# Kernel tuning notes

Measured on AMD Instinct MI355X. Metric: run time of the kernel, lower is better.

Reference implementation:

```python
import jax, jax.numpy as jnp
import numpy as np

N = 50000      # nodes
E = 800000     # edges (avg degree 16)
G = 256        # graphs in batch
IN = 128       # in_channels
H = 256        # hidden_channels
L = 4          # num_layers


def setup_inputs() -> dict:
    key = jax.random.key(0)
    ks = jax.random.split(key, 16)
    x = jax.random.normal(ks[0], (N, IN), dtype=jnp.float32)
    edge_index = jax.random.randint(ks[1], (2, E), 0, N, dtype=jnp.int64)
    batch = jnp.sort(jax.random.randint(ks[2], (N,), 0, G, dtype=jnp.int64))
    s_in = 1.0 / np.sqrt(IN)
    s_h = 1.0 / np.sqrt(H)
    return {
        "x": x,
        "edge_index": edge_index,
        "batch": batch,
        "w1_0": jax.random.normal(ks[3], (IN, H), jnp.float32) * s_in,
        "b1_0": jnp.zeros((H,), jnp.float32),
        "w2_0": jax.random.normal(ks[4], (H, H), jnp.float32) * s_h,
        "b2_0": jnp.zeros((H,), jnp.float32),
        "w1s": jax.random.normal(ks[5], (L - 1, H, H), jnp.float32) * s_h,
        "b1s": jnp.zeros((L - 1, H), jnp.float32),
        "w2s": jax.random.normal(ks[6], (L - 1, H, H), jnp.float32) * s_h,
        "b2s": jnp.zeros((L - 1, H), jnp.float32),
    }


def reference(x, edge_index, batch, w1_0, b1_0, w2_0, b2_0, w1s, b1s, w2s, b2s):
    n_nodes = x.shape[0]
    src, dst = edge_index[0], edge_index[1]

    def gin_layer(h, w1, b1, w2, b2):
        # scatter-add neighbor aggregation: out[i] = sum_{(j->i)} h[j]
        agg = jax.ops.segment_sum(h[src], dst, num_segments=n_nodes)
        z = h + agg  # GIN with eps = 0: (1+eps)*x + aggr
        z = jax.nn.relu(z @ w1 + b1) @ w2 + b2  # MLP: Linear-ReLU-Linear
        return jax.nn.relu(z)  # outer F.relu in forward

    h = gin_layer(x, w1_0, b1_0, w2_0, b2_0)
    for i in range(L - 1):  # small fixed layer loop
        h = gin_layer(h, w1s[i], b1s[i], w2s[i], b2s[i])

    # global_add_pool: per-graph segment sum -> [G, H]
    return jax.ops.segment_sum(h, batch, num_segments=G)
```

## Files before the change

### kernel.cpp

```cpp
#include <hip/hip_runtime.h>
#include <hip/hip_bf16.h>

#define NN 50000
#define NE 800000
#define NG 256
#define CIN 128
#define CH 256
#define CAP 64

typedef unsigned short u16;
typedef unsigned int u32;
typedef unsigned char u8;
typedef __attribute__((ext_vector_type(8))) short short8;
typedef __attribute__((ext_vector_type(8))) unsigned short ushort8;
typedef __attribute__((ext_vector_type(4))) float f32x4;

__device__ __forceinline__ float bf2f(u16 u) { return __uint_as_float(((u32)u) << 16); }
__device__ __forceinline__ u16 f2bf(float f) {
    u32 u = __float_as_uint(f);
    return (u16)((u + 0x7fffu + ((u >> 16) & 1u)) >> 16);
}

__global__ void k_prep(const float* __restrict__ x, u16* __restrict__ xb,
                       const float* __restrict__ w1_0, const float* __restrict__ w2_0,
                       const float* __restrict__ w1s, const float* __restrict__ w2s,
                       u16* __restrict__ Wp, int* __restrict__ deg,
                       float* __restrict__ outf,
                       float* __restrict__ S0, float* __restrict__ S1) {
    int t = blockIdx.x * 256 + threadIdx.x;
    if (t < NN) deg[t] = 0;
    if (t < NG * CH) outf[t] = 0.f;
    if (t < CIN) xb[(size_t)NN * CIN + t] = 0;
    if (t == 0) { S0[NN] = 0.f; S1[NN] = 0.f; }
    if (t < NN * CIN / 4) {
        float4 v = ((const float4*)x)[t];
        ushort4 o; o.x = f2bf(v.x); o.y = f2bf(v.y); o.z = f2bf(v.z); o.w = f2bf(v.w);
        ((ushort4*)xb)[t] = o;
    }
    if (t < CIN * CH + 7 * CH * CH) {
        const float* Wsrc; int rem;
        if (t < CIN * CH) { Wsrc = w1_0; rem = t; }
        else {
            int o = t - CIN * CH;
            int m = o >> 16; rem = o & 65535;
            Wsrc = (m == 0) ? w2_0
                 : (m <= 3) ? w1s + (size_t)(m - 1) * 65536
                            : w2s + (size_t)(m - 4) * 65536;
        }
        int j = rem & 7, lane = (rem >> 3) & 63, nt = (rem >> 9) & 15, kb = rem >> 13;
        int k = kb * 32 + ((lane >> 4) << 3) + j;
        int nc = nt * 16 + (lane & 15);
        Wp[t] = f2bf(Wsrc[k * CH + nc]);
    }
}

__global__ __launch_bounds__(256) void k_build(const int* __restrict__ dst,
                                               const int* __restrict__ src,
                                               int* __restrict__ deg,
                                               u16* __restrict__ colu) {
    int t = blockIdx.x * 256 + threadIdx.x;
    int e0 = t * 2;
    if (e0 < NE) {
        int2 d2 = *(const int2*)(dst + e0);
        int2 s2 = *(const int2*)(src + e0);
        int p0 = atomicAdd(&deg[d2.x], 1);
        int p1 = atomicAdd(&deg[d2.y], 1);
        colu[d2.x * CAP + p0] = (u16)s2.x;
        colu[d2.y * CAP + p1] = (u16)s2.y;
    }
}

#define ZS 264
template <int K1, bool QIN, bool QOUT, bool POOL>
__global__ __launch_bounds__(256, 6) void k_layer(const u16* __restrict__ G,
                                                  const int* __restrict__ deg,
                                                  const u16* __restrict__ colu,
                                                  const u8* __restrict__ Qin,
                                                  const float* __restrict__ Sin,
                                                  const u16* __restrict__ Wp1,
                                                  const float* __restrict__ b1,
                                                  const u16* __restrict__ Wp2,
                                                  const float* __restrict__ b2,
                                                  u16* __restrict__ out,
                                                  u8* __restrict__ Qout,
                                                  float* __restrict__ Sout,
                                                  const int* __restrict__ batchp,
                                                  float* __restrict__ outf) {
    __shared__ __align__(16) u16 zs[32 * ZS];
    const int tid = threadIdx.x;
    const int wave = tid >> 6, lane = tid & 63;
    const int quad = lane >> 4, l16 = lane & 15;
    const int m0 = blockIdx.x * 32;

    if (!QIN) {
        constexpr int LPR = K1 / 8;
        constexpr int RPG = 64 / LPR;
        const int sub = lane / LPR;
        const int c0 = (lane % LPR) * 8;
        for (int g = 0; g < 8; g += RPG) {
            int lr = wave * 8 + g + sub;
            int r = m0 + lr; if (r >= NN) r = NN - 1;
            const u16* base = G + c0;
            float a[8];
            ushort8 sv = *(const ushort8*)(base + (size_t)r * K1);
#pragma unroll
            for (int i = 0; i < 8; i++) a[i] = bf2f(sv[i]);
            int dg = deg[r];
            const u16* cb = colu + r * CAP;
            for (int e = 0; e < dg; e += 8) {
                ushort8 cv = *(const ushort8*)(cb + e);
                int idx[8];
#pragma unroll
                for (int u = 0; u < 8; u++)
                    idx[u] = (e + u < dg) ? (int)cv[u] : NN;
                ushort8 v[8];
#pragma unroll
                for (int u = 0; u < 8; u++)
                    v[u] = *(const ushort8*)(base + (size_t)idx[u] * K1);
#pragma unroll
                for (int u = 0; u < 8; u++)
#pragma unroll
                    for (int i = 0; i < 8; i++) a[i] += bf2f(v[u][i]);
            }
            ushort8 o;
#pragma unroll
            for (int i = 0; i < 8; i++) o[i] = f2bf(a[i]);
            *(ushort8*)(zs + lr * ZS + c0) = o;
        }
    } else {
        const int sub = lane >> 4;
        const int c0 = (lane & 15) * 16;
        for (int g = 0; g < 8; g += 4) {
            int lr = wave * 8 + g + sub;
            int r = m0 + lr; if (r >= NN) r = NN - 1;
            float a[16];
            const u16* sp = G + (size_t)r * CH + c0;
            ushort8 s0v = *(const ushort8*)sp;
            ushort8 s1v = *(const ushort8*)(sp + 8);
#pragma unroll
            for (int i = 0; i < 8; i++) { a[i] = bf2f(s0v[i]); a[8 + i] = bf2f(s1v[i]); }
            int dg = deg[r];
            const u16* cb = colu + r * CAP;
            for (int e = 0; e < dg; e += 4) {
                ushort4 cv = *(const ushort4*)(cb + e);
                int idx[4] = {(int)cv.x, (int)cv.y, (int)cv.z, (int)cv.w};
#pragma unroll
                for (int u = 0; u < 4; u++)
                    if (e + u >= dg) idx[u] = NN;
                uint4 qv[4]; float sc[4];
#pragma unroll
                for (int u = 0; u < 4; u++) {
                    qv[u] = *(const uint4*)(Qin + (size_t)idx[u] * CH + c0);
                    sc[u] = Sin[idx[u]];
                }
#pragma unroll
                for (int u = 0; u < 4; u++) {
#pragma unroll
                    for (int d = 0; d < 4; d++) {
                        u32 w = ((const u32*)&qv[u])[d];
                        a[d * 4 + 0] += sc[u] * (float)(w & 0xffu);
                        a[d * 4 + 1] += sc[u] * (float)((w >> 8) & 0xffu);
                        a[d * 4 + 2] += sc[u] * (float)((w >> 16) & 0xffu);
                        a[d * 4 + 3] += sc[u] * (float)(w >> 24);
                    }
                }
            }
            ushort8 o0, o1;
#pragma unroll
            for (int i = 0; i < 8; i++) { o0[i] = f2bf(a[i]); o1[i] = f2bf(a[8 + i]); }
            *(ushort8*)(zs + lr * ZS + c0) = o0;
            *(ushort8*)(zs + lr * ZS + c0 + 8) = o1;
        }
    }
    __syncthreads();

    f32x4 acc[2][4];
#pragma unroll
    for (int ri = 0; ri < 2; ri++)
#pragma unroll
        for (int nj = 0; nj < 4; nj++) acc[ri][nj] = (f32x4){0.f, 0.f, 0.f, 0.f};

    const u16* w1b = Wp1 + (wave * 4) * 512 + lane * 8;
    const u16* w2b = Wp2 + (wave * 4) * 512 + lane * 8;
    constexpr int KB1 = K1 / 32;
    short8 b_cur[4], b_nxt[4];
#pragma unroll
    for (int nj = 0; nj < 4; nj++) b_cur[nj] = *(const short8*)(w1b + nj * 512);

#pragma unroll
    for (int kb = 0; kb < KB1; kb++) {
        int kn = (kb + 1 < KB1) ? (kb + 1) : kb;
#pragma unroll
        for (int nj = 0; nj < 4; nj++)
            b_nxt[nj] = *(const short8*)(w1b + kn * 8192 + nj * 512);
        short8 a[2];
#pragma unroll
        for (int ri = 0; ri < 2; ri++)
            a[ri] = *(const short8*)(zs + (ri * 16 + l16) * ZS + kb * 32 + quad * 8);
#pragma unroll
        for (int nj = 0; nj < 4; nj++)
#pragma unroll
            for (int ri = 0; ri < 2; ri++)
                acc[ri][nj] = __builtin_amdgcn_mfma_f32_16x16x32_bf16(a[ri], b_cur[nj], acc[ri][nj], 0, 0, 0);
#pragma unroll
        for (int nj = 0; nj < 4; nj++) b_cur[nj] = b_nxt[nj];
    }

    short8 b2_cur[4];
#pragma unroll
    for (int nj = 0; nj < 4; nj++) b2_cur[nj] = *(const short8*)(w2b + nj * 512);

    __syncthreads();

#pragma unroll
    for (int nj = 0; nj < 4; nj++) {
        int cc = wave * 64 + nj * 16 + l16;
        float bv = b1[cc];
#pragma unroll
        for (int ri = 0; ri < 2; ri++) {
            f32x4 v = acc[ri][nj];
#pragma unroll
            for (int j = 0; j < 4; j++)
                zs[(ri * 16 + quad * 4 + j) * ZS + cc] = f2bf(fmaxf(v[j] + bv, 0.f));
        }
    }
    __syncthreads();

#pragma unroll
    for (int ri = 0; ri < 2; ri++)
#pragma unroll
        for (int nj = 0; nj < 4; nj++) acc[ri][nj] = (f32x4){0.f, 0.f, 0.f, 0.f};

#pragma unroll
    for (int kb = 0; kb < 8; kb++) {
        int kn = (kb + 1 < 8) ? (kb + 1) : kb;
#pragma unroll
        for (int nj = 0; nj < 4; nj++)
            b_nxt[nj] = *(const short8*)(w2b + kn * 8192 + nj * 512);
        short8 a[2];
#pragma unroll
        for (int ri = 0; ri < 2; ri++)
            a[ri] = *(const short8*)(zs + (ri * 16 + l16) * ZS + kb * 32 + quad * 8);
#pragma unroll
        for (int nj = 0; nj < 4; nj++)
#pragma unroll
            for (int ri = 0; ri < 2; ri++)
                acc[ri][nj] = __builtin_amdgcn_mfma_f32_16x16x32_bf16(a[ri], b2_cur[nj], acc[ri][nj], 0, 0, 0);
#pragma unroll
        for (int nj = 0; nj < 4; nj++) b2_cur[nj] = b_nxt[nj];
    }
    __syncthreads();

#pragma unroll
    for (int nj = 0; nj < 4; nj++) {
        int cc = wave * 64 + nj * 16 + l16;
        float bv = b2[cc];
#pragma unroll
        for (int ri = 0; ri < 2; ri++) {
            f32x4 v = acc[ri][nj];
#pragma unroll
            for (int j = 0; j < 4; j++)
                zs[(ri * 16 + quad * 4 + j) * ZS + cc] = f2bf(fmaxf(v[j] + bv, 0.f));
        }
    }
    __syncthreads();

    if (!POOL) {
        int row = tid >> 3, cb = (tid & 7) * 32;
        int r = m0 + row;
        if (r < NN) {
            uint4* dst = (uint4*)(out + (size_t)r * CH + cb);
            const u16* srcp = zs + row * ZS + cb;
#pragma unroll
            for (int c = 0; c < 4; c++) dst[c] = *(const uint4*)(srcp + c * 8);
            if (QOUT) {
                float vloc[32]; float mx = 0.f;
#pragma unroll
                for (int c = 0; c < 32; c++) { vloc[c] = bf2f(srcp[c]); mx = fmaxf(mx, vloc[c]); }
                mx = fmaxf(mx, __shfl_xor(mx, 1));
                mx = fmaxf(mx, __shfl_xor(mx, 2));
                mx = fmaxf(mx, __shfl_xor(mx, 4));
                float inv = mx > 0.f ? 255.f / mx : 0.f;
                u32 qw[8];
#pragma unroll
                for (int d = 0; d < 8; d++) {
                    u32 q0 = (u32)(vloc[d * 4 + 0] * inv + 0.5f);
                    u32 q1 = (u32)(vloc[d * 4 + 1] * inv + 0.5f);
                    u32 q2 = (u32)(vloc[d * 4 + 2] * inv + 0.5f);
                    u32 q3 = (u32)(vloc[d * 4 + 3] * inv + 0.5f);
                    qw[d] = q0 | (q1 << 8) | (q2 << 16) | (q3 << 24);
                }
                uint4* qdst = (uint4*)(Qout + (size_t)r * CH + cb);
                qdst[0] = *(const uint4*)&qw[0];
                qdst[1] = *(const uint4*)&qw[4];
                if ((tid & 7) == 0) Sout[r] = mx * (1.f / 255.f);
            }
        }
    } else {
        int c = tid;
        float acc2 = 0.f;
        int cur_g = batchp[m0];
        for (int row = 0; row < 32; row++) {
            int r = m0 + row;
            if (r >= NN) break;
            int g = batchp[r];
            if (g != cur_g) {
                atomicAdd(&outf[cur_g * CH + c], acc2);
                acc2 = 0.f; cur_g = g;
            }
            acc2 += bf2f(zs[row * ZS + c]);
        }
        atomicAdd(&outf[cur_g * CH + c], acc2);
    }
}

extern "C" void kernel_launch(void* const* d_in, const int* in_sizes, int n_in,
                              void* d_out, int out_size, void* d_ws, size_t ws_size,
                              hipStream_t stream) {
    const float* x     = (const float*)d_in[0];
    const int*   ei    = (const int*)d_in[1];
    const int*   batch = (const int*)d_in[2];
    const float* w1_0  = (const float*)d_in[3];
    const float* b1_0  = (const float*)d_in[4];
    const float* w2_0  = (const float*)d_in[5];
    const float* b2_0  = (const float*)d_in[6];
    const float* w1s   = (const float*)d_in[7];
    const float* b1s   = (const float*)d_in[8];
    const float* w2s   = (const float*)d_in[9];
    const float* b2s   = (const float*)d_in[10];
    float* out = (float*)d_out;

    char* p = (char*)d_ws;
    u16* Hb  = (u16*)p; p += (size_t)(NN + 1) * CH * 2;
    u16* Tb  = (u16*)p; p += (size_t)(NN + 1) * CH * 2;
    u16* xb  = (u16*)p; p += (size_t)(NN + 1) * CIN * 2;
    u16* WpA = (u16*)p; p += (size_t)(CIN * CH + 7 * CH * CH) * 2;
    int* deg = (int*)p; p += (size_t)NN * 4;
    u16* colu= (u16*)p; p += (size_t)NN * CAP * 2;
    u8*  Q0  = (u8*)p;  p += (size_t)(NN + 1) * CH;
    u8*  Q1  = (u8*)p;  p += (size_t)(NN + 1) * CH;
    float* S0 = (float*)p; p += (size_t)(NN + 1) * 4;
    float* S1 = (float*)p; p += (size_t)(NN + 1) * 4;

    u16* Wp1_0 = WpA;
    u16* Wp2_0 = Wp1_0 + CIN * CH;
    u16* Wp1sA = Wp2_0 + CH * CH;
    u16* Wp2sA = Wp1sA + 3 * CH * CH;

    const int* srcv = ei;
    const int* dstv = ei + NE;

    hipLaunchKernelGGL(k_prep, dim3((NN * CIN / 4 + 255) / 256), dim3(256), 0, stream,
                       x, xb, w1_0, w2_0, w1s, w2s, WpA, deg, out, S0, S1);

    hipLaunchKernelGGL(k_build, dim3((NE / 2 + 255) / 256), dim3(256), 0, stream,
                       dstv, srcv, deg, colu);

    int layerBlocks = (NN + 31) / 32;

    hipLaunchKernelGGL((k_layer<128, false, true, false>), dim3(layerBlocks), dim3(256), 0, stream,
                       xb, deg, colu, (const u8*)nullptr, (const float*)nullptr,
                       Wp1_0, b1_0, Wp2_0, b2_0, Hb, Q0, S0, batch, out);
    hipLaunchKernelGGL((k_layer<256, true, true, false>), dim3(layerBlocks), dim3(256), 0, stream,
                       Hb, deg, colu, Q0, S0,
                       Wp1sA, b1s, Wp2sA, b2s, Tb, Q1, S1, batch, out);
    hipLaunchKernelGGL((k_layer<256, true, true, false>), dim3(layerBlocks), dim3(256), 0, stream,
                       Tb, deg, colu, Q1, S1,
                       Wp1sA + (size_t)CH * CH, b1s + CH,
                       Wp2sA + (size_t)CH * CH, b2s + CH, Hb, Q0, S0, batch, out);
    hipLaunchKernelGGL((k_layer<256, true, false, true>), dim3(layerBlocks), dim3(256), 0, stream,
                       Hb, deg, colu, Q0, S0,
                       Wp1sA + (size_t)2 * CH * CH, b1s + 2 * CH,
                       Wp2sA + (size_t)2 * CH * CH, b2s + 2 * CH,
                       (u16*)nullptr, (u8*)nullptr, (float*)nullptr, batch, out);
}
```

Before: 393.8 us.

## Bucket neighbor lists by source range and prefetch slices for cache locality

Adds a k_sort pass that reorders each node's neighbor list into 8 source-node partitions and stores packed per-partition prefix counts. The gather loops in k_layer then walk the partitions in lockstep across all blocks, while each block prefetches a slice of the upcoming partitions' feature rows. The goal is to keep the random gathers within a cache-resident window instead of touching the whole feature table at once. This costs an extra kernel launch, redundant prefetch loads with hardcoded offsets, and processes two rows interleaved per lane, which raises register pressure.

Measured after the change: 561.3 us. 1.43x slower.

```diff
diff --git a/kernel.cpp b/kernel.cpp
--- a/kernel.cpp
+++ b/kernel.cpp
@@ -7,18 +7,32 @@
 #define CIN 128
 #define CH 256
 #define CAP 64
+#define NPART 8
 
 typedef unsigned short u16;
 typedef unsigned int u32;
 typedef unsigned char u8;
+typedef unsigned long long u64;
 typedef __attribute__((ext_vector_type(8))) short short8;
 typedef __attribute__((ext_vector_type(8))) unsigned short ushort8;
 typedef __attribute__((ext_vector_type(4))) float f32x4;
+typedef __attribute__((ext_vector_type(4))) unsigned int u32x4;
 
 __device__ __forceinline__ float bf2f(u16 u) { return __uint_as_float(((u32)u) << 16); }
 __device__ __forceinline__ u16 f2bf(float f) {
     u32 u = __float_as_uint(f);
     return (u16)((u + 0x7fffu + ((u >> 16) & 1u)) >> 16);
+}
+
+__device__ __forceinline__ void pf_slice(const u8* base, int p, int islice, int tid) {
+    size_t off = (size_t)p * 1600000 + (size_t)islice * 8192 + (size_t)tid * 32;
+    const size_t lim = 12800224;
+    if (off > lim) off = lim;
+    const u32x4* q = (const u32x4*)(base + off);
+    u32x4 v0 = q[0];
+    u32x4 v1 = q[1];
+    u32 s = v0[0] ^ v0[1] ^ v0[2] ^ v0[3] ^ v1[0] ^ v1[1] ^ v1[2] ^ v1[3];
+    asm volatile("" :: "v"(s));
 }
 
 __global__ void k_prep(const float* __restrict__ x, u16* __restrict__ xb,
@@ -70,11 +84,35 @@
     }
 }
 
+__global__ __launch_bounds__(256) void k_sort(const int* __restrict__ deg,
+                                              u16* __restrict__ colu,
+                                              u64* __restrict__ cnt) {
+    const int lane = threadIdx.x & 63;
+    const int r = blockIdx.x * 4 + (threadIdx.x >> 6);
+    if (r >= NN) return;
+    const int dg = deg[r];
+    const bool valid = lane < dg;
+    u16 id = colu[r * CAP + lane];
+    u32 p = valid ? (u32)(((u64)id * 687195ull) >> 32) : 8u;
+    const u64 lm = (1ull << lane) - 1;
+    int base = 0, mypos = 0;
+    u64 packed = 0;
+#pragma unroll
+    for (u32 q = 0; q < 8; q++) {
+        u64 m = __ballot(p == q);
+        if (p == q) mypos = base + __popcll(m & lm);
+        base += __popcll(m);
+        packed |= ((u64)(u32)base) << (q * 8);
+    }
+    if (valid) colu[r * CAP + mypos] = id;
+    if (lane == 0) cnt[r] = packed;
+}
+
 #define ZS 264
 template <int K1, bool QIN, bool QOUT, bool POOL>
 __global__ __launch_bounds__(256, 6) void k_layer(const u16* __restrict__ G,
-                                                  const int* __restrict__ deg,
                                                   const u16* __restrict__ colu,
+                                                  const u64* __restrict__ cnt,
                                                   const u8* __restrict__ Qin,
                                                   const float* __restrict__ Sin,
                                                   const u16* __restrict__ Wp1,
@@ -91,83 +129,122 @@
     const int wave = tid >> 6, lane = tid & 63;
     const int quad = lane >> 4, l16 = lane & 15;
     const int m0 = blockIdx.x * 32;
+    const int islice = (int)blockIdx.x >> 3;
 
     if (!QIN) {
         constexpr int LPR = K1 / 8;
         constexpr int RPG = 64 / LPR;
         const int sub = lane / LPR;
         const int c0 = (lane % LPR) * 8;
-        for (int g = 0; g < 8; g += RPG) {
-            int lr = wave * 8 + g + sub;
+        int ee[2]; u64 cn[2];
+        const u16* cbp[2];
+        float a[2][8];
+#pragma unroll
+        for (int b = 0; b < 2; b++) {
+            int lr = wave * 8 + b * RPG + sub;
             int r = m0 + lr; if (r >= NN) r = NN - 1;
-            const u16* base = G + c0;
-            float a[8];
-            ushort8 sv = *(const ushort8*)(base + (size_t)r * K1);
-#pragma unroll
-            for (int i = 0; i < 8; i++) a[i] = bf2f(sv[i]);
-            int dg = deg[r];
-            const u16* cb = colu + r * CAP;
-            for (int e = 0; e < dg; e += 8) {
-                ushort8 cv = *(const ushort8*)(cb + e);
-                int idx[8];
-#pragma unroll
-                for (int u = 0; u < 8; u++)
-                    idx[u] = (e + u < dg) ? (int)cv[u] : NN;
-                ushort8 v[8];
-#pragma unroll
-                for (int u = 0; u < 8; u++)
-                    v[u] = *(const ushort8*)(base + (size_t)idx[u] * K1);
-#pragma unroll
-                for (int u = 0; u < 8; u++)
-#pragma unroll
-                    for (int i = 0; i < 8; i++) a[i] += bf2f(v[u][i]);
+            ee[b] = 0; cbp[b] = colu + r * CAP; cn[b] = cnt[r];
+            ushort8 sv = *(const ushort8*)(G + (size_t)r * K1 + c0);
+#pragma unroll
+            for (int i = 0; i < 8; i++) a[b][i] = bf2f(sv[i]);
+        }
+        const u8* pfb = (const u8*)G;
+        pf_slice(pfb, 0, islice, tid);
+        pf_slice(pfb, 1, islice, tid);
+        const u16* base = G + c0;
+        for (int p = 0; p < 8; p++) {
+            if (p < 6) pf_slice(pfb, p + 2, islice, tid);
+#pragma unroll
+            for (int b = 0; b < 2; b++) {
+                const int limit = (int)((cn[b] >> (p * 8)) & 0xffu);
+                const int dgt = (int)(cn[b] >> 56);
+                while (ee[b] < limit) {
+                    int e = ee[b];
+                    ushort8 cv = *(const ushort8*)(cbp[b] + e);
+                    int idx[8];
+#pragma unroll
+                    for (int u = 0; u < 8; u++)
+                        idx[u] = (e + u < dgt) ? (int)cv[u] : NN;
+                    ushort8 v[8];
+#pragma unroll
+                    for (int u = 0; u < 8; u++)
+                        v[u] = *(const ushort8*)(base + (size_t)idx[u] * K1);
+#pragma unroll
+                    for (int u = 0; u < 8; u++)
+#pragma unroll
+                        for (int i = 0; i < 8; i++) a[b][i] += bf2f(v[u][i]);
+                    ee[b] = e + 8;
+                }
             }
+        }
+#pragma unroll
+        for (int b = 0; b < 2; b++) {
+            int lr = wave * 8 + b * RPG + sub;
             ushort8 o;
 #pragma unroll
-            for (int i = 0; i < 8; i++) o[i] = f2bf(a[i]);
+            for (int i = 0; i < 8; i++) o[i] = f2bf(a[b][i]);
             *(ushort8*)(zs + lr * ZS + c0) = o;
         }
     } else {
         const int sub = lane >> 4;
         const int c0 = (lane & 15) * 16;
-        for (int g = 0; g < 8; g += 4) {
-            int lr = wave * 8 + g + sub;
+        int ee[2]; u64 cn[2];
+        const u16* cbp[2];
+        float a[2][16];
+#pragma unroll
+        for (int b = 0; b < 2; b++) {
+            int lr = wave * 8 + b * 4 + sub;
             int r = m0 + lr; if (r >= NN) r = NN - 1;
-            float a[16];
+            ee[b] = 0; cbp[b] = colu + r * CAP; cn[b] = cnt[r];
             const u16* sp = G + (size_t)r * CH + c0;
             ushort8 s0v = *(const ushort8*)sp;
             ushort8 s1v = *(const ushort8*)(sp + 8);
 #pragma unroll
-            for (int i = 0; i < 8; i++) { a[i] = bf2f(s0v[i]); a[8 + i] = bf2f(s1v[i]); }
-            int dg = deg[r];
-            const u16* cb = colu + r * CAP;
-            for (int e = 0; e < dg; e += 4) {
-                ushort4 cv = *(const ushort4*)(cb + e);
-                int idx[4] = {(int)cv.x, (int)cv.y, (int)cv.z, (int)cv.w};
-#pragma unroll
-                for (int u = 0; u < 4; u++)
-                    if (e + u >= dg) idx[u] = NN;
-                uint4 qv[4]; float sc[4];
-#pragma unroll
-                for (int u = 0; u < 4; u++) {
-                    qv[u] = *(const uint4*)(Qin + (size_t)idx[u] * CH + c0);
-                    sc[u] = Sin[idx[u]];
-                }
-#pragma unroll
-                for (int u = 0; u < 4; u++) {
-#pragma unroll
-                    for (int d = 0; d < 4; d++) {
-                        u32 w = ((const u32*)&qv[u])[d];
-                        a[d * 4 + 0] += sc[u] * (float)(w & 0xffu);
-                        a[d * 4 + 1] += sc[u] * (float)((w >> 8) & 0xffu);
-                        a[d * 4 + 2] += sc[u] * (float)((w >> 16) & 0xffu);
-                        a[d * 4 + 3] += sc[u] * (float)(w >> 24);
+            for (int i = 0; i < 8; i++) { a[b][i] = bf2f(s0v[i]); a[b][8 + i] = bf2f(s1v[i]); }
+        }
+        const u8* pfb = Qin;
+        pf_slice(pfb, 0, islice, tid);
+        pf_slice(pfb, 1, islice, tid);
+        for (int p = 0; p < 8; p++) {
+            if (p < 6) pf_slice(pfb, p + 2, islice, tid);
+#pragma unroll
+            for (int b = 0; b < 2; b++) {
+                const int limit = (int)((cn[b] >> (p * 8)) & 0xffu);
+                const int dgt = (int)(cn[b] >> 56);
+                while (ee[b] < limit) {
+                    int e = ee[b];
+                    ushort4 cv = *(const ushort4*)(cbp[b] + e);
+                    int idx[4] = {(int)cv.x, (int)cv.y, (int)cv.z, (int)cv.w};
+#pragma unroll
+                    for (int u = 0; u < 4; u++)
+                        if (e + u >= dgt) idx[u] = NN;
+                    uint4 qv[4]; float sc[4];
+#pragma unroll
+                    for (int u = 0; u < 4; u++) {
+                        qv[u] = *(const uint4*)(Qin + (size_t)idx[u] * CH + c0);
+                        sc[u] = Sin[idx[u]];
                     }
+#pragma unroll
+                    for (int u = 0; u < 4; u++) {
+#pragma unroll
+                        for (int d = 0; d < 4; d++) {
+                            u32 w = ((const u32*)&qv[u])[d];
+                            a[b][d * 4 + 0] += sc[u] * (float)(w & 0xffu);
+                            a[b][d * 4 + 1] += sc[u] * (float)((w >> 8) & 0xffu);
+                            a[b][d * 4 + 2] += sc[u] * (float)((w >> 16) & 0xffu);
+                            a[b][d * 4 + 3] += sc[u] * (float)(w >> 24);
+                        }
+                    }
+                    ee[b] = e + 4;
                 }
             }
+        }
+#pragma unroll
+        for (int b = 0; b < 2; b++) {
+            int lr = wave * 8 + b * 4 + sub;
             ushort8 o0, o1;
 #pragma unroll
-            for (int i = 0; i < 8; i++) { o0[i] = f2bf(a[i]); o1[i] = f2bf(a[8 + i]); }
+            for (int i = 0; i < 8; i++) { o0[i] = f2bf(a[b][i]); o1[i] = f2bf(a[b][8 + i]); }
             *(ushort8*)(zs + lr * ZS + c0) = o0;
             *(ushort8*)(zs + lr * ZS + c0 + 8) = o1;
         }
@@ -339,6 +416,7 @@
     u16* colu= (u16*)p; p += (size_t)NN * CAP * 2;
     u8*  Q0  = (u8*)p;  p += (size_t)(NN + 1) * CH;
     u8*  Q1  = (u8*)p;  p += (size_t)(NN + 1) * CH;
+    u64* cnt = (u64*)p; p += (size_t)NN * 8;
     float* S0 = (float*)p; p += (size_t)(NN + 1) * 4;
     float* S1 = (float*)p; p += (size_t)(NN + 1) * 4;
 
@@ -356,20 +434,23 @@
     hipLaunchKernelGGL(k_build, dim3((NE / 2 + 255) / 256), dim3(256), 0, stream,
                        dstv, srcv, deg, colu);
 
+    hipLaunchKernelGGL(k_sort, dim3(NN / 4), dim3(256), 0, stream,
+                       deg, colu, cnt);
+
     int layerBlocks = (NN + 31) / 32;
 
     hipLaunchKernelGGL((k_layer<128, false, true, false>), dim3(layerBlocks), dim3(256), 0, stream,
-                       xb, deg, colu, (const u8*)nullptr, (const float*)nullptr,
+                       xb, colu, cnt, (const u8*)nullptr, (const float*)nullptr,
                        Wp1_0, b1_0, Wp2_0, b2_0, Hb, Q0, S0, batch, out);
     hipLaunchKernelGGL((k_layer<256, true, true, false>), dim3(layerBlocks), dim3(256), 0, stream,
-                       Hb, deg, colu, Q0, S0,
+                       Hb, colu, cnt, Q0, S0,
                        Wp1sA, b1s, Wp2sA, b2s, Tb, Q1, S1, batch, out);
     hipLaunchKernelGGL((k_layer<256, true, true, false>), dim3(layerBlocks), dim3(256), 0, stream,
-                       Tb, deg, colu, Q1, S1,
+                       Tb, colu, cnt, Q1, S1,
                        Wp1sA + (size_t)CH * CH, b1s + CH,
                        Wp2sA + (size_t)CH * CH, b2s + CH, Hb, Q0, S0, batch, out);
     hipLaunchKernelGGL((k_layer<256, true, false, true>), dim3(layerBlocks), dim3(256), 0, stream,
-                       Hb, deg, colu, Q0, S0,
+                       Hb, colu, cnt, Q0, S0,
                        Wp1sA + (size_t)2 * CH * CH, b1s + 2 * CH,
                        Wp2sA + (size_t)2 * CH * CH, b2s + 2 * CH,
                        (u16*)nullptr, (u8*)nullptr, (float*)nullptr, batch, out);
```

## Warp-specialize layer kernel: producer waves gather while consumer waves run MLP

Applied to the files above, without the earlier changes.

Each 512-thread block handles three 32-row tiles in sequence. Four producer waves gather neighbor aggregates into a double-buffered shared tile, while four consumer waves run the two MFMA GEMMs and the epilogue on the previous tile. The aim is to overlap the latency-bound gather with the matrix compute. In exchange the grid shrinks to 521 blocks with fewer resident blocks per CU, producer and consumer barrier counts must stay matched, and the block count is hardcoded.

Result: slower. 835.5 us (+112.2%).

```diff
diff --git a/kernel.cpp b/kernel.cpp
--- a/kernel.cpp
+++ b/kernel.cpp
@@ -71,8 +71,9 @@
 }
 
 #define ZS 264
+#define ZT (32 * ZS)
 template <int K1, bool QIN, bool QOUT, bool POOL>
-__global__ __launch_bounds__(256, 6) void k_layer(const u16* __restrict__ G,
+__global__ __launch_bounds__(512, 4) void k_layer(const u16* __restrict__ G,
                                                   const int* __restrict__ deg,
                                                   const u16* __restrict__ colu,
                                                   const u8* __restrict__ Qin,
@@ -86,231 +87,244 @@
                                                   float* __restrict__ Sout,
                                                   const int* __restrict__ batchp,
                                                   float* __restrict__ outf) {
-    __shared__ __align__(16) u16 zs[32 * ZS];
+    __shared__ __align__(16) u16 zs[2 * ZT];
     const int tid = threadIdx.x;
     const int wave = tid >> 6, lane = tid & 63;
     const int quad = lane >> 4, l16 = lane & 15;
-    const int m0 = blockIdx.x * 32;
-
-    if (!QIN) {
-        constexpr int LPR = K1 / 8;
-        constexpr int RPG = 64 / LPR;
-        const int sub = lane / LPR;
-        const int c0 = (lane % LPR) * 8;
-        for (int g = 0; g < 8; g += RPG) {
-            int lr = wave * 8 + g + sub;
-            int r = m0 + lr; if (r >= NN) r = NN - 1;
-            const u16* base = G + c0;
-            float a[8];
-            ushort8 sv = *(const ushort8*)(base + (size_t)r * K1);
-#pragma unroll
-            for (int i = 0; i < 8; i++) a[i] = bf2f(sv[i]);
-            int dg = deg[r];
-            const u16* cb = colu + r * CAP;
-            for (int e = 0; e < dg; e += 8) {
-                ushort8 cv = *(const ushort8*)(cb + e);
-                int idx[8];
-#pragma unroll
-                for (int u = 0; u < 8; u++)
-                    idx[u] = (e + u < dg) ? (int)cv[u] : NN;
-                ushort8 v[8];
-#pragma unroll
-                for (int u = 0; u < 8; u++)
-                    v[u] = *(const ushort8*)(base + (size_t)idx[u] * K1);
-#pragma unroll
-                for (int u = 0; u < 8; u++)
-#pragma unroll
-                    for (int i = 0; i < 8; i++) a[i] += bf2f(v[u][i]);
-            }
-            ushort8 o;
-#pragma unroll
-            for (int i = 0; i < 8; i++) o[i] = f2bf(a[i]);
-            *(ushort8*)(zs + lr * ZS + c0) = o;
+    const bool isP = wave < 4;
+    const int cw = isP ? 0 : wave - 4;
+    const int ctid = isP ? 0 : tid - 256;
+    const u16* w1b = Wp1 + (cw * 4) * 512 + lane * 8;
+    const u16* w2b = Wp2 + (cw * 4) * 512 + lane * 8;
+
+    for (int t = 0; t <= 3; ++t) {
+        if (isP) {
+            if (t < 3) {
+                u16* zb = zs + (t & 1) * ZT;
+                const int m0 = (blockIdx.x * 3 + t) * 32;
+                const int pw = wave;
+                if (!QIN) {
+                    constexpr int LPR = K1 / 8;
+                    constexpr int RPG = 64 / LPR;
+                    const int sub = lane / LPR;
+                    const int c0 = (lane % LPR) * 8;
+                    for (int g = 0; g < 8; g += RPG) {
+                        int lr = pw * 8 + g + sub;
+                        int r = m0 + lr; if (r >= NN) r = NN - 1;
+                        const u16* base = G + c0;
+                        float a[8];
+                        ushort8 sv = *(const ushort8*)(base + (size_t)r * K1);
+#pragma unroll
+                        for (int i = 0; i < 8; i++) a[i] = bf2f(sv[i]);
+                        int dg = deg[r];
+                        const u16* cb = colu + r * CAP;
+                        for (int e = 0; e < dg; e += 8) {
+                            ushort8 cv = *(const ushort8*)(cb + e);
+                            int idx[8];
+#pragma unroll
+                            for (int u = 0; u < 8; u++)
+                                idx[u] = (e + u < dg) ? (int)cv[u] : NN;
+                            ushort8 v[8];
+#pragma unroll
+                            for (int u = 0; u < 8; u++)
+                                v[u] = *(const ushort8*)(base + (size_t)idx[u] * K1);
+#pragma unroll
+                            for (int u = 0; u < 8; u++)
+#pragma unroll
+                                for (int i = 0; i < 8; i++) a[i] += bf2f(v[u][i]);
+                        }
+                        ushort8 o;
+#pragma unroll
+                        for (int i = 0; i < 8; i++) o[i] = f2bf(a[i]);
+                        *(ushort8*)(zb + lr * ZS + c0) = o;
+                    }
+                } else {
+                    const int sub = lane >> 4;
+                    const int c0 = (lane & 15) * 16;
+                    for (int g = 0; g < 8; g += 4) {
+                        int lr = pw * 8 + g + sub;
+                        int r = m0 + lr; if (r >= NN) r = NN - 1;
+                        float a[16];
+                        const u16* sp = G + (size_t)r * CH + c0;
+                        ushort8 s0v = *(const ushort8*)sp;
+                        ushort8 s1v = *(const ushort8*)(sp + 8);
+#pragma unroll
+                        for (int i = 0; i < 8; i++) { a[i] = bf2f(s0v[i]); a[8 + i] = bf2f(s1v[i]); }
+                        int dg = deg[r];
+                        const u16* cb = colu + r * CAP;
+                        for (int e = 0; e < dg; e += 4) {
+                            ushort4 cv = *(const ushort4*)(cb + e);
+                            int idx[4] = {(int)cv.x, (int)cv.y, (int)cv.z, (int)cv.w};
+#pragma unroll
+                            for (int u = 0; u < 4; u++)
+                                if (e + u >= dg) idx[u] = NN;
+                            uint4 qv[4]; float sc[4];
+#pragma unroll
+                            for (int u = 0; u < 4; u++) {
+                                qv[u] = *(const uint4*)(Qin + (size_t)idx[u] * CH + c0);
+                                sc[u] = Sin[idx[u]];
+                            }
+#pragma unroll
+                            for (int u = 0; u < 4; u++) {
+#pragma unroll
+                                for (int d = 0; d < 4; d++) {
+                                    u32 w = ((const u32*)&qv[u])[d];
+                                    a[d * 4 + 0] += sc[u] * (float)(w & 0xffu);
+                                    a[d * 4 + 1] += sc[u] * (float)((w >> 8) & 0xffu);
+                                    a[d * 4 + 2] += sc[u] * (float)((w >> 16) & 0xffu);
+                                    a[d * 4 + 3] += sc[u] * (float)(w >> 24);
+                                }
+                            }
+                        }
+                        ushort8 o0, o1;
+#pragma unroll
+                        for (int i = 0; i < 8; i++) { o0[i] = f2bf(a[i]); o1[i] = f2bf(a[8 + i]); }
+                        *(ushort8*)(zb + lr * ZS + c0) = o0;
+                        *(ushort8*)(zb + lr * ZS + c0 + 8) = o1;
+                    }
+                }
+            }
+            __syncthreads(); __syncthreads(); __syncthreads(); __syncthreads();
+        } else if (t >= 1) {
+            u16* zb = zs + ((t - 1) & 1) * ZT;
+            const int m0 = (blockIdx.x * 3 + (t - 1)) * 32;
+
+            f32x4 acc[2][4];
+#pragma unroll
+            for (int ri = 0; ri < 2; ri++)
+#pragma unroll
+                for (int nj = 0; nj < 4; nj++) acc[ri][nj] = (f32x4){0.f, 0.f, 0.f, 0.f};
+            constexpr int KB1 = K1 / 32;
+            short8 b_cur[4], b_nxt[4];
+#pragma unroll
+            for (int nj = 0; nj < 4; nj++) b_cur[nj] = *(const short8*)(w1b + nj * 512);
+#pragma unroll
+            for (int kb = 0; kb < KB1; kb++) {
+                int kn = (kb + 1 < KB1) ? (kb + 1) : kb;
+#pragma unroll
+                for (int nj = 0; nj < 4; nj++)
+                    b_nxt[nj] = *(const short8*)(w1b + kn * 8192 + nj * 512);
+                short8 a[2];
+#pragma unroll
+                for (int ri = 0; ri < 2; ri++)
+                    a[ri] = *(const short8*)(zb + (ri * 16 + l16) * ZS + kb * 32 + quad * 8);
+#pragma unroll
+                for (int nj = 0; nj < 4; nj++)
+#pragma unroll
+                    for (int ri = 0; ri < 2; ri++)
+                        acc[ri][nj] = __builtin_amdgcn_mfma_f32_16x16x32_bf16(a[ri], b_cur[nj], acc[ri][nj], 0, 0, 0);
+#pragma unroll
+                for (int nj = 0; nj < 4; nj++) b_cur[nj] = b_nxt[nj];
+            }
+            short8 b2_cur[4];
+#pragma unroll
+            for (int nj = 0; nj < 4; nj++) b2_cur[nj] = *(const short8*)(w2b + nj * 512);
+
+            __syncthreads();
+
+#pragma unroll
+            for (int nj = 0; nj < 4; nj++) {
+                int cc = cw * 64 + nj * 16 + l16;
+                float bv = b1[cc];
+#pragma unroll
+                for (int ri = 0; ri < 2; ri++) {
+                    f32x4 v = acc[ri][nj];
+#pragma unroll
+                    for (int j = 0; j < 4; j++)
+                        zb[(ri * 16 + quad * 4 + j) * ZS + cc] = f2bf(fmaxf(v[j] + bv, 0.f));
+                }
+            }
+            __syncthreads();
+
+#pragma unroll
+            for (int ri = 0; ri < 2; ri++)
+#pragma unroll
+                for (int nj = 0; nj < 4; nj++) acc[ri][nj] = (f32x4){0.f, 0.f, 0.f, 0.f};
+#pragma unroll
+            for (int kb = 0; kb < 8; kb++) {
+                int kn = (kb + 1 < 8) ? (kb + 1) : kb;
+#pragma unroll
+                for (int nj = 0; nj < 4; nj++)
+                    b_nxt[nj] = *(const short8*)(w2b + kn * 8192 + nj * 512);
+                short8 a[2];
+#pragma unroll
+                for (int ri = 0; ri < 2; ri++)
+                    a[ri] = *(const short8*)(zb + (ri * 16 + l16) * ZS + kb * 32 + quad * 8);
+#pragma unroll
+                for (int nj = 0; nj < 4; nj++)
+#pragma unroll
+                    for (int ri = 0; ri < 2; ri++)
+                        acc[ri][nj] = __builtin_amdgcn_mfma_f32_16x16x32_bf16(a[ri], b2_cur[nj], acc[ri][nj], 0, 0, 0);
+#pragma unroll
+                for (int nj = 0; nj < 4; nj++) b2_cur[nj] = b_nxt[nj];
+            }
+            __syncthreads();
+
+#pragma unroll
+            for (int nj = 0; nj < 4; nj++) {
+                int cc = cw * 64 + nj * 16 + l16;
+                float bv = b2[cc];
+#pragma unroll
+                for (int ri = 0; ri < 2; ri++) {
+                    f32x4 v = acc[ri][nj];
+#pragma unroll
+                    for (int j = 0; j < 4; j++)
+                        zb[(ri * 16 + quad * 4 + j) * ZS + cc] = f2bf(fmaxf(v[j] + bv, 0.f));
+                }
+            }
+            __syncthreads();
+
+            if (!POOL) {
+                int row = ctid >> 3, cb = (ctid & 7) * 32;
+                int r = m0 + row;
+                if (r < NN) {
+                    uint4* dst = (uint4*)(out + (size_t)r * CH + cb);
+                    const u16* srcp = zb + row * ZS + cb;
+#pragma unroll
+                    for (int c = 0; c < 4; c++) dst[c] = *(const uint4*)(srcp + c * 8);
+                    if (QOUT) {
+                        float vloc[32]; float mx = 0.f;
+#pragma unroll
+                        for (int c = 0; c < 32; c++) { vloc[c] = bf2f(srcp[c]); mx = fmaxf(mx, vloc[c]); }
+                        mx = fmaxf(mx, __shfl_xor(mx, 1));
+                        mx = fmaxf(mx, __shfl_xor(mx, 2));
+                        mx = fmaxf(mx, __shfl_xor(mx, 4));
+                        float inv = mx > 0.f ? 255.f / mx : 0.f;
+                        u32 qw[8];
+#pragma unroll
+                        for (int d = 0; d < 8; d++) {
+                            u32 q0 = (u32)(vloc[d * 4 + 0] * inv + 0.5f);
+                            u32 q1 = (u32)(vloc[d * 4 + 1] * inv + 0.5f);
+                            u32 q2 = (u32)(vloc[d * 4 + 2] * inv + 0.5f);
+                            u32 q3 = (u32)(vloc[d * 4 + 3] * inv + 0.5f);
+                            qw[d] = q0 | (q1 << 8) | (q2 << 16) | (q3 << 24);
+                        }
+                        uint4* qdst = (uint4*)(Qout + (size_t)r * CH + cb);
+                        qdst[0] = *(const uint4*)&qw[0];
+                        qdst[1] = *(const uint4*)&qw[4];
+                        if ((ctid & 7) == 0) Sout[r] = mx * (1.f / 255.f);
+                    }
+                }
+            } else {
+                int c = ctid;
+                float acc2 = 0.f;
+                int cur_g = batchp[m0];
+                for (int row = 0; row < 32; row++) {
+                    int r = m0 + row;
+                    if (r >= NN) break;
+                    int g = batchp[r];
+                    if (g != cur_g) {
+                        atomicAdd(&outf[cur_g * CH + c], acc2);
+                        acc2 = 0.f; cur_g = g;
+                    }
+                    acc2 += bf2f(zb[row * ZS + c]);
+                }
+                atomicAdd(&outf[cur_g * CH + c], acc2);
+            }
+        } else {
+            __syncthreads(); __syncthreads(); __syncthreads(); __syncthreads();
         }
-    } else {
-        const int sub = lane >> 4;
-        const int c0 = (lane & 15) * 16;
-        for (int g = 0; g < 8; g += 4) {
-            int lr = wave * 8 + g + sub;
-            int r = m0 + lr; if (r >= NN) r = NN - 1;
-            float a[16];
-            const u16* sp = G + (size_t)r * CH + c0;
-            ushort8 s0v = *(const ushort8*)sp;
-            ushort8 s1v = *(const ushort8*)(sp + 8);
-#pragma unroll
-            for (int i = 0; i < 8; i++) { a[i] = bf2f(s0v[i]); a[8 + i] = bf2f(s1v[i]); }
-            int dg = deg[r];
-            const u16* cb = colu + r * CAP;
-            for (int e = 0; e < dg; e += 4) {
-                ushort4 cv = *(const ushort4*)(cb + e);
-                int idx[4] = {(int)cv.x, (int)cv.y, (int)cv.z, (int)cv.w};
-#pragma unroll
-                for (int u = 0; u < 4; u++)
-                    if (e + u >= dg) idx[u] = NN;
-                uint4 qv[4]; float sc[4];
-#pragma unroll
-                for (int u = 0; u < 4; u++) {
-                    qv[u] = *(const uint4*)(Qin + (size_t)idx[u] * CH + c0);
-                    sc[u] = Sin[idx[u]];
-                }
-#pragma unroll
-                for (int u = 0; u < 4; u++) {
-#pragma unroll
-                    for (int d = 0; d < 4; d++) {
-                        u32 w = ((const u32*)&qv[u])[d];
-                        a[d * 4 + 0] += sc[u] * (float)(w & 0xffu);
-                        a[d * 4 + 1] += sc[u] * (float)((w >> 8) & 0xffu);
-                        a[d * 4 + 2] += sc[u] * (float)((w >> 16) & 0xffu);
-                        a[d * 4 + 3] += sc[u] * (float)(w >> 24);
-                    }
-                }
-            }
-            ushort8 o0, o1;
-#pragma unroll
-            for (int i = 0; i < 8; i++) { o0[i] = f2bf(a[i]); o1[i] = f2bf(a[8 + i]); }
-            *(ushort8*)(zs + lr * ZS + c0) = o0;
-            *(ushort8*)(zs + lr * ZS + c0 + 8) = o1;
-        }
-    }
-    __syncthreads();
-
-    f32x4 acc[2][4];
-#pragma unroll
-    for (int ri = 0; ri < 2; ri++)
-#pragma unroll
-        for (int nj = 0; nj < 4; nj++) acc[ri][nj] = (f32x4){0.f, 0.f, 0.f, 0.f};
-
-    const u16* w1b = Wp1 + (wave * 4) * 512 + lane * 8;
-    const u16* w2b = Wp2 + (wave * 4) * 512 + lane * 8;
-    constexpr int KB1 = K1 / 32;
-    short8 b_cur[4], b_nxt[4];
-#pragma unroll
-    for (int nj = 0; nj < 4; nj++) b_cur[nj] = *(const short8*)(w1b + nj * 512);
-
-#pragma unroll
-    for (int kb = 0; kb < KB1; kb++) {
-        int kn = (kb + 1 < KB1) ? (kb + 1) : kb;
-#pragma unroll
-        for (int nj = 0; nj < 4; nj++)
-            b_nxt[nj] = *(const short8*)(w1b + kn * 8192 + nj * 512);
-        short8 a[2];
-#pragma unroll
-        for (int ri = 0; ri < 2; ri++)
-            a[ri] = *(const short8*)(zs + (ri * 16 + l16) * ZS + kb * 32 + quad * 8);
-#pragma unroll
-        for (int nj = 0; nj < 4; nj++)
-#pragma unroll
-            for (int ri = 0; ri < 2; ri++)
-                acc[ri][nj] = __builtin_amdgcn_mfma_f32_16x16x32_bf16(a[ri], b_cur[nj], acc[ri][nj], 0, 0, 0);
-#pragma unroll
-        for (int nj = 0; nj < 4; nj++) b_cur[nj] = b_nxt[nj];
-    }
-
-    short8 b2_cur[4];
-#pragma unroll
-    for (int nj = 0; nj < 4; nj++) b2_cur[nj] = *(const short8*)(w2b + nj * 512);
-
-    __syncthreads();
-
-#pragma unroll
-    for (int nj = 0; nj < 4; nj++) {
-        int cc = wave * 64 + nj * 16 + l16;
-        float bv = b1[cc];
-#pragma unroll
-        for (int ri = 0; ri < 2; ri++) {
-            f32x4 v = acc[ri][nj];
-#pragma unroll
-            for (int j = 0; j < 4; j++)
-                zs[(ri * 16 + quad * 4 + j) * ZS + cc] = f2bf(fmaxf(v[j] + bv, 0.f));
-        }
-    }
-    __syncthreads();
-
-#pragma unroll
-    for (int ri = 0; ri < 2; ri++)
-#pragma unroll
-        for (int nj = 0; nj < 4; nj++) acc[ri][nj] = (f32x4){0.f, 0.f, 0.f, 0.f};
-
-#pragma unroll
-    for (int kb = 0; kb < 8; kb++) {
-        int kn = (kb + 1 < 8) ? (kb + 1) : kb;
-#pragma unroll
-        for (int nj = 0; nj < 4; nj++)
-            b_nxt[nj] = *(const short8*)(w2b + kn * 8192 + nj * 512);
-        short8 a[2];
-#pragma unroll
-        for (int ri = 0; ri < 2; ri++)
-            a[ri] = *(const short8*)(zs + (ri * 16 + l16) * ZS + kb * 32 + quad * 8);
-#pragma unroll
-        for (int nj = 0; nj < 4; nj++)
-#pragma unroll
-            for (int ri = 0; ri < 2; ri++)
-                acc[ri][nj] = __builtin_amdgcn_mfma_f32_16x16x32_bf16(a[ri], b2_cur[nj], acc[ri][nj], 0, 0, 0);
-#pragma unroll
-        for (int nj = 0; nj < 4; nj++) b2_cur[nj] = b_nxt[nj];
-    }
-    __syncthreads();
-
-#pragma unroll
-    for (int nj = 0; nj < 4; nj++) {
-        int cc = wave * 64 + nj * 16 + l16;
-        float bv = b2[cc];
-#pragma unroll
-        for (int ri = 0; ri < 2; ri++) {
-            f32x4 v = acc[ri][nj];
-#pragma unroll
-            for (int j = 0; j < 4; j++)
-                zs[(ri * 16 + quad * 4 + j) * ZS + cc] = f2bf(fmaxf(v[j] + bv, 0.f));
-        }
-    }
-    __syncthreads();
-
-    if (!POOL) {
-        int row = tid >> 3, cb = (tid & 7) * 32;
-        int r = m0 + row;
-        if (r < NN) {
-            uint4* dst = (uint4*)(out + (size_t)r * CH + cb);
-            const u16* srcp = zs + row * ZS + cb;
-#pragma unroll
-            for (int c = 0; c < 4; c++) dst[c] = *(const uint4*)(srcp + c * 8);
-            if (QOUT) {
-                float vloc[32]; float mx = 0.f;
-#pragma unroll
-                for (int c = 0; c < 32; c++) { vloc[c] = bf2f(srcp[c]); mx = fmaxf(mx, vloc[c]); }
-                mx = fmaxf(mx, __shfl_xor(mx, 1));
-                mx = fmaxf(mx, __shfl_xor(mx, 2));
-                mx = fmaxf(mx, __shfl_xor(mx, 4));
-                float inv = mx > 0.f ? 255.f / mx : 0.f;
-                u32 qw[8];
-#pragma unroll
-                for (int d = 0; d < 8; d++) {
-                    u32 q0 = (u32)(vloc[d * 4 + 0] * inv + 0.5f);
-                    u32 q1 = (u32)(vloc[d * 4 + 1] * inv + 0.5f);
-                    u32 q2 = (u32)(vloc[d * 4 + 2] * inv + 0.5f);
-                    u32 q3 = (u32)(vloc[d * 4 + 3] * inv + 0.5f);
-                    qw[d] = q0 | (q1 << 8) | (q2 << 16) | (q3 << 24);
-                }
-                uint4* qdst = (uint4*)(Qout + (size_t)r * CH + cb);
-                qdst[0] = *(const uint4*)&qw[0];
-                qdst[1] = *(const uint4*)&qw[4];
-                if ((tid & 7) == 0) Sout[r] = mx * (1.f / 255.f);
-            }
-        }
-    } else {
-        int c = tid;
-        float acc2 = 0.f;
-        int cur_g = batchp[m0];
-        for (int row = 0; row < 32; row++) {
-            int r = m0 + row;
-            if (r >= NN) break;
-            int g = batchp[r];
-            if (g != cur_g) {
-                atomicAdd(&outf[cur_g * CH + c], acc2);
-                acc2 = 0.f; cur_g = g;
-            }
-            acc2 += bf2f(zs[row * ZS + c]);
-        }
-        atomicAdd(&outf[cur_g * CH + c], acc2);
+        __syncthreads();
     }
 }
 
@@ -356,19 +370,19 @@
     hipLaunchKernelGGL(k_build, dim3((NE / 2 + 255) / 256), dim3(256), 0, stream,
                        dstv, srcv, deg, colu);
 
-    int layerBlocks = (NN + 31) / 32;
-
-    hipLaunchKernelGGL((k_layer<128, false, true, false>), dim3(layerBlocks), dim3(256), 0, stream,
+    int layerBlocks = 521;
+
+    hipLaunchKernelGGL((k_layer<128, false, true, false>), dim3(layerBlocks), dim3(512), 0, stream,
                        xb, deg, colu, (const u8*)nullptr, (const float*)nullptr,
                        Wp1_0, b1_0, Wp2_0, b2_0, Hb, Q0, S0, batch, out);
-    hipLaunchKernelGGL((k_layer<256, true, true, false>), dim3(layerBlocks), dim3(256), 0, stream,
+    hipLaunchKernelGGL((k_layer<256, true, true, false>), dim3(layerBlocks), dim3(512), 0, stream,
                        Hb, deg, colu, Q0, S0,
                        Wp1sA, b1s, Wp2sA, b2s, Tb, Q1, S1, batch, out);
-    hipLaunchKernelGGL((k_layer<256, true, true, false>), dim3(layerBlocks), dim3(256), 0, stream,
+    hipLaunchKernelGGL((k_layer<256, true, true, false>), dim3(layerBlocks), dim3(512), 0, stream,
                        Tb, deg, colu, Q1, S1,
                        Wp1sA + (size_t)CH * CH, b1s + CH,
                        Wp2sA + (size_t)CH * CH, b2s + CH, Hb, Q0, S0, batch, out);
-    hipLaunchKernelGGL((k_layer<256, true, false, true>), dim3(layerBlocks), dim3(256), 0, stream,
+    hipLaunchKernelGGL((k_layer<256, true, false, true>), dim3(layerBlocks), dim3(512), 0, stream,
                        Hb, deg, colu, Q0, S0,
                        Wp1sA + (size_t)2 * CH * CH, b1s + 2 * CH,
                        Wp2sA + (size_t)2 * CH * CH, b2s + 2 * CH,
```
